# Performance work log

Measured on AMD Instinct MI355X. Metric: run time of the kernel, lower is better.

Reference implementation:

```python
import jax, jax.numpy as jnp
import numpy as np

STRIDE = 1
PADDING = 1


def setup_inputs() -> dict:
    key = jax.random.key(0)
    k1, k2, k3 = jax.random.split(key, 3)
    x = jax.random.normal(k1, (16, 64, 224, 224), dtype=jnp.float32)
    W = jax.random.normal(k2, (64, 64, 3, 3), dtype=jnp.float32)
    b = jax.random.normal(k3, (64,), dtype=jnp.float32)
    return {"x": x, "W": W, "b": b}


def reference(x, W, b):
    # Equivalent of the naive im2col+GEMM conv: a standard 2D convolution
    # (cross-correlation) with stride/padding, NCHW layout, OIHW weights.
    out = jax.lax.conv_general_dilated(
        x, W,
        window_strides=(STRIDE, STRIDE),
        padding=[(PADDING, PADDING), (PADDING, PADDING)],
        dimension_numbers=("NCHW", "OIHW", "NCHW"),
    )
    return out + b[None, :, None, None]
```

## Files before the change

### kernel.cpp

```cpp
#include <hip/hip_runtime.h>
#include <hip/hip_bf16.h>


typedef __attribute__((ext_vector_type(8)))  short   short8;
typedef __attribute__((ext_vector_type(8)))  unsigned short ushort8;
typedef __attribute__((ext_vector_type(16))) float   float16_t;

#define HW (224 * 224)

__device__ __forceinline__ unsigned short f2bf(float f) {
  __hip_bfloat16 h = __float2bfloat16(f);
  return *reinterpret_cast<unsigned short*>(&h);
}

__global__ void build_wt(const float* __restrict__ W, unsigned short* __restrict__ wt) {
  int i = blockIdx.x * 256 + threadIdx.x;
  if (i < 9 * 64 * 64) {
    int tap = i >> 12;
    int rem = i & 4095;
    int nn  = rem >> 6;
    int c   = rem & 63;
    wt[i] = f2bf(W[(nn * 64 + c) * 9 + tap]);
  }
}

__global__ __launch_bounds__(512, 4) void conv3x3_mfma(
    const float* __restrict__ x, const unsigned short* __restrict__ wt,
    const float* __restrict__ bias, float* __restrict__ out) {
  __shared__ __align__(16) unsigned short xs[18 * 8 * 34 * 8];

  const int w0  = blockIdx.x * 32;
  const int h0  = blockIdx.y * 16;
  const int img = blockIdx.z;
  const int tid = threadIdx.x;
  const int lane = tid & 63, wave = tid >> 6;
  const int ln31 = lane & 31, lhi = lane >> 5;

  const float* xn = x + (size_t)img * 64 * HW;

  for (int i = tid; i < 18 * 8 * 34; i += 512) {
    int h   = i / (8 * 34);
    int rem = i - h * (8 * 34);
    int cg  = rem / 34;
    int w   = rem - cg * 34;
    int gh = h0 - 1 + h;
    int gw = w0 - 1 + w;
    ushort8 pk;
    if ((unsigned)gh < 224u && (unsigned)gw < 224u) {
      const float* p = xn + (size_t)cg * 8 * HW + gh * 224 + gw;
#pragma unroll
      for (int j = 0; j < 8; ++j) pk[j] = f2bf(p[(size_t)j * HW]);
    } else {
#pragma unroll
      for (int j = 0; j < 8; ++j) pk[j] = 0;
    }
    *reinterpret_cast<ushort8*>(&xs[i * 8]) = pk;
  }
  __syncthreads();

  const int row0 = wave * 2;
  float16_t acc[2][2];
#pragma unroll
  for (int rb = 0; rb < 2; ++rb)
#pragma unroll
    for (int nb = 0; nb < 2; ++nb) acc[rb][nb] = 0.f;

#pragma unroll
  for (int r = 0; r < 3; ++r) {
#pragma unroll
    for (int s = 0; s < 3; ++s) {
      const int tap = r * 3 + s;
#pragma unroll
      for (int ks = 0; ks < 4; ++ks) {
        const short8 b0 = *reinterpret_cast<const short8*>(
            wt + ((tap * 64 + 0 * 32 + ln31) * 64 + ks * 16 + lhi * 8));
        const short8 b1 = *reinterpret_cast<const short8*>(
            wt + ((tap * 64 + 1 * 32 + ln31) * 64 + ks * 16 + lhi * 8));
        const int cg = ks * 2 + lhi;
#pragma unroll
        for (int rb = 0; rb < 2; ++rb) {
          const int hidx = row0 + rb + r;
          const int widx = ln31 + s;
          const short8 a = *reinterpret_cast<const short8*>(
              &xs[(((hidx * 8) + cg) * 34 + widx) * 8]);
          acc[rb][0] = __builtin_amdgcn_mfma_f32_32x32x16_bf16(b0, a, acc[rb][0], 0, 0, 0);
          acc[rb][1] = __builtin_amdgcn_mfma_f32_32x32x16_bf16(b1, a, acc[rb][1], 0, 0, 0);
        }
      }
    }
  }

#pragma unroll
  for (int rb = 0; rb < 2; ++rb) {
    const int h = h0 + row0 + rb;
#pragma unroll
    for (int nb = 0; nb < 2; ++nb) {
#pragma unroll
      for (int q = 0; q < 4; ++q) {
#pragma unroll
        for (int j = 0; j < 4; ++j) {
          const int m  = j + 8 * q + 4 * lhi;
          const int ch = nb * 32 + m;
          const float v = acc[rb][nb][4 * q + j] + bias[ch];
          out[(((size_t)img * 64 + ch) * 224 + h) * 224 + w0 + ln31] = v;
        }
      }
    }
  }
}

#define TW 32
#define TH 32
#define KB 16
#define PXT 4
__global__ __launch_bounds__(256) void conv3x3_direct(
    const float* __restrict__ x, const float* __restrict__ wgt,
    const float* __restrict__ bias, float* __restrict__ out) {
  __shared__ float xsf[34 * 35];
  const int tx = blockIdx.x % 7, ty = blockIdx.x / 7;
  const int k0 = blockIdx.y * KB, n = blockIdx.z;
  const int w0 = tx * TW, h0 = ty * TH;
  const int tid = threadIdx.x;
  const int tw = tid & 7, th = tid >> 3;
  float acc[KB][PXT];
#pragma unroll
  for (int k = 0; k < KB; ++k)
#pragma unroll
    for (int p = 0; p < PXT; ++p) acc[k][p] = 0.f;
  const float* xn = x + (size_t)n * 64 * HW;
  for (int c = 0; c < 64; ++c) {
    const float* xc = xn + (size_t)c * HW;
    for (int i = tid; i < 34 * 34; i += 256) {
      int row = i / 34, col = i - row * 34;
      int gh = h0 - 1 + row, gw = w0 - 1 + col;
      float v = 0.f;
      if (gh >= 0 && gh < 224 && gw >= 0 && gw < 224) v = xc[gh * 224 + gw];
      xsf[row * 35 + col] = v;
    }
    __syncthreads();
    float in[3][6];
#pragma unroll
    for (int r = 0; r < 3; ++r)
#pragma unroll
      for (int q = 0; q < 6; ++q) in[r][q] = xsf[(th + r) * 35 + tw * PXT + q];
    const float* wc = wgt + ((size_t)k0 * 64 + c) * 9;
#pragma unroll
    for (int k = 0; k < KB; ++k) {
      const float* wk = wc + (size_t)k * 64 * 9;
#pragma unroll
      for (int r = 0; r < 3; ++r)
#pragma unroll
        for (int s = 0; s < 3; ++s) {
          float wv = wk[r * 3 + s];
#pragma unroll
          for (int p = 0; p < PXT; ++p) acc[k][p] += wv * in[r][s + p];
        }
    }
    __syncthreads();
  }
#pragma unroll
  for (int k = 0; k < KB; ++k) {
    float bv = bias[k0 + k];
    float4 v = make_float4(acc[k][0] + bv, acc[k][1] + bv, acc[k][2] + bv, acc[k][3] + bv);
    float* op = out + ((((size_t)n * 64 + (k0 + k)) * 224 + (h0 + th)) * 224 + (w0 + tw * PXT));
    *reinterpret_cast<float4*>(op) = v;
  }
}

extern "C" void kernel_launch(void* const* d_in, const int* in_sizes, int n_in,
                              void* d_out, int out_size, void* d_ws, size_t ws_size,
                              hipStream_t stream) {
  const float* x = (const float*)d_in[0];
  const float* W = (const float*)d_in[1];
  const float* b = (const float*)d_in[2];
  float* out = (float*)d_out;

  if (ws_size >= 9 * 64 * 64 * sizeof(unsigned short)) {
    unsigned short* wt = (unsigned short*)d_ws;
    build_wt<<<144, 256, 0, stream>>>(W, wt);
    dim3 grid(7, 14, 16);
    conv3x3_mfma<<<grid, 512, 0, stream>>>(x, wt, b, out);
  } else {
    dim3 grid(7 * 7, 64 / KB, 16);
    conv3x3_direct<<<grid, 256, 0, stream>>>(x, W, b, out);
  }
}
```

Before: 506.0 us.

## Retile MFMA conv to full-width two-row strips with split channel staging

```diff
diff --git a/kernel.cpp b/kernel.cpp
--- a/kernel.cpp
+++ b/kernel.cpp
@@ -24,86 +24,98 @@
   }
 }
 
-__global__ __launch_bounds__(512, 4) void conv3x3_mfma(
+__global__ __launch_bounds__(448, 4) void conv3x3_mfma(
     const float* __restrict__ x, const unsigned short* __restrict__ wt,
     const float* __restrict__ bias, float* __restrict__ out) {
-  __shared__ __align__(16) unsigned short xs[18 * 8 * 34 * 8];
+  __shared__ __align__(16) unsigned short xs[4 * 4 * 226 * 8];
 
-  const int w0  = blockIdx.x * 32;
-  const int h0  = blockIdx.y * 16;
-  const int img = blockIdx.z;
+  const int bid = blockIdx.x;
+  const int t   = (bid & 7) * 224 + (bid >> 3);
+  const int ht  = t % 112;
+  const int img = t / 112;
+  const int h0  = ht * 2;
+
   const int tid = threadIdx.x;
   const int lane = tid & 63, wave = tid >> 6;
   const int ln31 = lane & 31, lhi = lane >> 5;
 
   const float* xn = x + (size_t)img * 64 * HW;
 
-  for (int i = tid; i < 18 * 8 * 34; i += 512) {
-    int h   = i / (8 * 34);
-    int rem = i - h * (8 * 34);
-    int cg  = rem / 34;
-    int w   = rem - cg * 34;
-    int gh = h0 - 1 + h;
-    int gw = w0 - 1 + w;
-    ushort8 pk;
-    if ((unsigned)gh < 224u && (unsigned)gw < 224u) {
-      const float* p = xn + (size_t)cg * 8 * HW + gh * 224 + gw;
-#pragma unroll
-      for (int j = 0; j < 8; ++j) pk[j] = f2bf(p[(size_t)j * HW]);
-    } else {
-#pragma unroll
-      for (int j = 0; j < 8; ++j) pk[j] = 0;
-    }
-    *reinterpret_cast<ushort8*>(&xs[i * 8]) = pk;
-  }
-  __syncthreads();
-
-  const int row0 = wave * 2;
   float16_t acc[2][2];
 #pragma unroll
-  for (int rb = 0; rb < 2; ++rb)
+  for (int mt2 = 0; mt2 < 2; ++mt2)
 #pragma unroll
-    for (int nb = 0; nb < 2; ++nb) acc[rb][nb] = 0.f;
+    for (int nb = 0; nb < 2; ++nb) acc[mt2][nb] = 0.f;
+
+  for (int half = 0; half < 2; ++half) {
+    for (int i = tid; i < 4 * 4 * 226; i += 448) {
+      const int hcg = i / 226;
+      const int w   = i - hcg * 226;
+      const int hl  = hcg >> 2;
+      const int cgl = hcg & 3;
+      const int gh  = h0 - 1 + hl;
+      const int gw  = w - 1;
+      ushort8 pk;
+      if (((unsigned)gh < 224u) && ((unsigned)gw < 224u)) {
+        const float* p = xn + (size_t)(half * 32 + cgl * 8) * HW + gh * 224 + gw;
+#pragma unroll
+        for (int j = 0; j < 8; ++j) pk[j] = f2bf(p[(size_t)j * HW]);
+      } else {
+#pragma unroll
+        for (int j = 0; j < 8; ++j) pk[j] = 0;
+      }
+      *reinterpret_cast<ushort8*>(&xs[i * 8]) = pk;
+    }
+    __syncthreads();
 
 #pragma unroll
-  for (int r = 0; r < 3; ++r) {
+    for (int ks = 0; ks < 2; ++ks) {
 #pragma unroll
-    for (int s = 0; s < 3; ++s) {
-      const int tap = r * 3 + s;
+      for (int r = 0; r < 3; ++r) {
 #pragma unroll
-      for (int ks = 0; ks < 4; ++ks) {
-        const short8 b0 = *reinterpret_cast<const short8*>(
-            wt + ((tap * 64 + 0 * 32 + ln31) * 64 + ks * 16 + lhi * 8));
-        const short8 b1 = *reinterpret_cast<const short8*>(
-            wt + ((tap * 64 + 1 * 32 + ln31) * 64 + ks * 16 + lhi * 8));
-        const int cg = ks * 2 + lhi;
+        for (int s = 0; s < 3; ++s) {
+          const int tap = r * 3 + s;
+          const short8 b0 = *reinterpret_cast<const short8*>(
+              wt + ((tap * 64 + ln31) * 64 + half * 32 + ks * 16 + lhi * 8));
+          const short8 b1 = *reinterpret_cast<const short8*>(
+              wt + ((tap * 64 + 32 + ln31) * 64 + half * 32 + ks * 16 + lhi * 8));
+          const int cgl = ks * 2 + lhi;
 #pragma unroll
-        for (int rb = 0; rb < 2; ++rb) {
-          const int hidx = row0 + rb + r;
-          const int widx = ln31 + s;
-          const short8 a = *reinterpret_cast<const short8*>(
-              &xs[(((hidx * 8) + cg) * 34 + widx) * 8]);
-          acc[rb][0] = __builtin_amdgcn_mfma_f32_32x32x16_bf16(b0, a, acc[rb][0], 0, 0, 0);
-          acc[rb][1] = __builtin_amdgcn_mfma_f32_32x32x16_bf16(b1, a, acc[rb][1], 0, 0, 0);
+          for (int mt2 = 0; mt2 < 2; ++mt2) {
+            const int mt = wave * 2 + mt2;
+            const int hh = mt / 7;
+            const int w0 = (mt - hh * 7) * 32;
+            const short8 a = *reinterpret_cast<const short8*>(
+                &xs[((((hh + r) * 4) + cgl) * 226 + (w0 + ln31 + s)) * 8]);
+            acc[mt2][0] = __builtin_amdgcn_mfma_f32_32x32x16_bf16(a, b0, acc[mt2][0], 0, 0, 0);
+            acc[mt2][1] = __builtin_amdgcn_mfma_f32_32x32x16_bf16(a, b1, acc[mt2][1], 0, 0, 0);
+          }
         }
       }
     }
+    if (half == 0) __syncthreads();
   }
 
 #pragma unroll
-  for (int rb = 0; rb < 2; ++rb) {
-    const int h = h0 + row0 + rb;
+  for (int mt2 = 0; mt2 < 2; ++mt2) {
+    const int mt = wave * 2 + mt2;
+    const int hh = mt / 7;
+    const int w0 = (mt - hh * 7) * 32;
+    const int h  = h0 + hh;
 #pragma unroll
     for (int nb = 0; nb < 2; ++nb) {
+      const int ch = nb * 32 + ln31;
+      const float bv = bias[ch];
+      float* op = out + (((size_t)img * 64 + ch) * 224 + h) * 224 + w0;
 #pragma unroll
       for (int q = 0; q < 4; ++q) {
-#pragma unroll
-        for (int j = 0; j < 4; ++j) {
-          const int m  = j + 8 * q + 4 * lhi;
-          const int ch = nb * 32 + m;
-          const float v = acc[rb][nb][4 * q + j] + bias[ch];
-          out[(((size_t)img * 64 + ch) * 224 + h) * 224 + w0 + ln31] = v;
-        }
+        const int wloc = 8 * q + 4 * lhi;
+        float4 v;
+        v.x = acc[mt2][nb][4 * q + 0] + bv;
+        v.y = acc[mt2][nb][4 * q + 1] + bv;
+        v.z = acc[mt2][nb][4 * q + 2] + bv;
+        v.w = acc[mt2][nb][4 * q + 3] + bv;
+        *reinterpret_cast<float4*>(op + wloc) = v;
       }
     }
   }
@@ -178,8 +190,7 @@
   if (ws_size >= 9 * 64 * 64 * sizeof(unsigned short)) {
     unsigned short* wt = (unsigned short*)d_ws;
     build_wt<<<144, 256, 0, stream>>>(W, wt);
-    dim3 grid(7, 14, 16);
-    conv3x3_mfma<<<grid, 512, 0, stream>>>(x, wt, b, out);
+    conv3x3_mfma<<<1792, 448, 0, stream>>>(x, wt, b, out);
   } else {
     dim3 grid(7 * 7, 64 / KB, 16);
     conv3x3_direct<<<grid, 256, 0, stream>>>(x, W, b, out);
```

New measurement: 478.2 us. 1.06x faster.
